# Performance work log

Hardware: AMD Instinct MI355X
Metric: run time of the kernel (lower is better)

Reference implementation:

```python
import jax, jax.numpy as jnp
import numpy as np

B, N, F_IN, F_OUT, H = 4, 2048, 64, 64, 4

def setup_inputs() -> dict:
    key = jax.random.key(0)
    k1, k2, k3, k4 = jax.random.split(key, 4)
    node_features = jax.random.normal(k1, (B, N, F_IN), dtype=jnp.float32)
    adj_matrix = jax.random.randint(k2, (B, N, N), 0, 2, dtype=jnp.int32)
    # nn.Linear(in, H*out, bias=False): stored here as [in, H*out] so y = x @ W
    W = jax.random.normal(k3, (F_IN, H * F_OUT), dtype=jnp.float32) * (1.0 / np.sqrt(F_IN))
    # per-head additive-attention vector over concatenated [h_i || h_j] (width 2*F_OUT)
    attention = jax.random.normal(k4, (H, 2 * F_OUT), dtype=jnp.float32) * 0.1
    return {"node_features": node_features, "adj_matrix": adj_matrix, "W": W, "attention": attention}

def reference(node_features, adj_matrix, W, attention):
    Bv, Nv = node_features.shape[0], node_features.shape[1]
    # h: [B, H, N, F_OUT]
    h = (node_features @ W).reshape(Bv, Nv, H, F_OUT).transpose(0, 2, 1, 3)
    # Additive GAT scores: a_h . [h_i || h_j] decomposed so the [B,H,N,N,2F] concat
    # tensor is never materialized (same math as concat + einsum in the source).
    a_src, a_dst = attention[:, :F_OUT], attention[:, F_OUT:]
    s_src = jnp.einsum('bhnf,hf->bhn', h, a_src)
    s_dst = jnp.einsum('bhnf,hf->bhn', h, a_dst)
    scores = s_src[:, :, :, None] + s_dst[:, :, None, :]          # [B,H,N,N]
    scores = jnp.where(scores >= 0, scores, 0.2 * scores)          # LeakyReLU(0.2)
    mask = adj_matrix[:, None, :, :].astype(bool)                  # [B,1,N,N]
    scores = jnp.where(mask, scores, -jnp.inf)                     # masked_fill(~mask, -inf)
    attn = jax.nn.softmax(scores, axis=-1)                         # softmax over neighbors j
    # dropout is identity in eval mode (deterministic reference)
    h_prime = jnp.einsum('bhij,bhjf->bhif', attn, h)               # weighted neighbor sum
    return h_prime.transpose(0, 2, 1, 3).reshape(Bv, Nv, H * F_OUT)
```

## Files before the change

kernel.cpp:

```cpp
#include <hip/hip_runtime.h>

#define NN 2048
#define NH 4
#define COLS 256

typedef __attribute__((ext_vector_type(8))) short short8;
typedef __attribute__((ext_vector_type(4))) float f32x4;
typedef __attribute__((ext_vector_type(4))) int i32x4;
typedef __attribute__((ext_vector_type(4))) unsigned u32x4;

__device__ __forceinline__ ushort f2bf(float x) {
  union { float f; unsigned u; } v; v.f = x;
  unsigned r = v.u + 0x7fffu + ((v.u >> 16) & 1u);
  return (ushort)(r >> 16);
}
__device__ __forceinline__ unsigned cvtpk(float lo, float hi) {
  unsigned r;
  asm("v_cvt_pk_bf16_f32 %0, %1, %2" : "=v"(r) : "v"(lo), "v"(hi));
  return r;
}
__device__ __forceinline__ unsigned pack16(i32x4 a, i32x4 b, i32x4 c, i32x4 d) {
  unsigned m = 0;
  #pragma unroll
  for (int e = 0; e < 4; ++e) {
    m |= (a[e] != 0 ? 1u : 0u) << e;
    m |= (b[e] != 0 ? 1u : 0u) << (e + 4);
    m |= (c[e] != 0 ? 1u : 0u) << (e + 8);
    m |= (d[e] != 0 ? 1u : 0u) << (e + 12);
  }
  return m;
}

__global__ __launch_bounds__(256) void k1_prep(
    const float* __restrict__ nf, const float* __restrict__ W,
    const float* __restrict__ att, ushort* __restrict__ hB,
    float* __restrict__ s_src, float* __restrict__ s_dst)
{
  const int tid = threadIdx.x;
  const int head = tid >> 6, lane = tid & 63;
  const int bid = blockIdx.x;

  float w[64];
  #pragma unroll
  for (int f = 0; f < 64; ++f) w[f] = W[f * COLS + tid];

  const float LOG2E = 1.4426950408889634f;
  const float asrc = att[head * 128 + lane] * LOG2E;
  const float adst = att[head * 128 + 64 + lane] * LOG2E;

  __shared__ float xs[512];
  __shared__ ushort st8[8 * 256];

  #pragma unroll 1
  for (int g = 0; g < 2; ++g) {
    const int m0 = bid * 16 + g * 8;
    __syncthreads();
    xs[tid]       = nf[m0 * 64 + tid];
    xs[tid + 256] = nf[m0 * 64 + 256 + tid];
    __syncthreads();

    #pragma unroll
    for (int rr = 0; rr < 8; ++rr) {
      float acc = 0.f;
      #pragma unroll
      for (int f = 0; f < 64; ++f) acc = fmaf(xs[rr * 64 + f], w[f], acc);
      st8[rr * 256 + tid] = f2bf(acc);
      float vs = acc * asrc, vd = acc * adst;
      #pragma unroll
      for (int off = 32; off > 0; off >>= 1) {
        vs += __shfl_xor(vs, off);
        vd += __shfl_xor(vd, off);
      }
      if (lane == 0) {
        const int m = m0 + rr;
        const int b = m >> 11, n = m & (NN - 1);
        s_src[(b * NH + head) * NN + n] = vs;
        s_dst[(b * NH + head) * NN + n] = vd;
      }
    }
    __syncthreads();
    {
      const int t = (tid >> 4) & 3, fl = tid & 15;
      const int col = head * 64 + t * 16 + fl;
      unsigned pk[4];
      #pragma unroll
      for (int e = 0; e < 4; ++e) {
        const unsigned lo = st8[(2 * e) * 256 + col];
        const unsigned hi = st8[(2 * e + 1) * 256 + col];
        pk[e] = lo | (hi << 16);
      }
      const int b   = m0 >> 11;
      const int jc  = (m0 & (NN - 1)) >> 5;
      const int grp = (m0 & 31) >> 3;
      const size_t chunk =
          (((size_t)(b * NH + head) * 64 + jc) * 4 + t) * 64 + (grp * 16 + fl);
      uint4 vv; vv.x = pk[0]; vv.y = pk[1]; vv.z = pk[2]; vv.w = pk[3];
      *(uint4*)(hB + chunk * 8) = vv;
    }
  }
}

__global__ __launch_bounds__(1024) void k2_main(
    const int* __restrict__ adj, const ushort* __restrict__ hB,
    const float* __restrict__ s_src, const float* __restrict__ s_dst,
    float* __restrict__ out)
{
  const int tid = threadIdx.x;
  const int wv  = tid >> 6;
  const int w   = wv >> 2;
  const int js  = wv & 3;
  const int l   = tid & 63;
  int bid = blockIdx.x;
  bid = (bid & 7) * 32 + (bid >> 3);
  const int b   = bid >> 6;
  const int i0  = (bid & 63) << 5;

  const int bh   = b * NH + w;
  const int r16  = l & 15;
  const int grp  = l >> 4;
  const int koff = grp << 3;

  const int sjs = tid >> 8, srow = (tid >> 3) & 31, soct = tid & 7;
  const int* sbase = adj + ((size_t)b * NN + i0 + srow) * NN + sjs * 512 + soct * 16;

  const float ssl = s_src[bh * NN + i0 + r16];
  const float ssh = s_src[bh * NN + i0 + 16 + r16];
  const float*  sdp = s_dst + bh * NN;
  const ushort* hbW = hB + (size_t)bh * 131072 + l * 8;

  __shared__ unsigned abits[2][4][32][4];
  __shared__ f32x4 red[NH][10][64];

  const short8 ones = {(short)0x3F80, (short)0x3F80, (short)0x3F80, (short)0x3F80,
                       (short)0x3F80, (short)0x3F80, (short)0x3F80, (short)0x3F80};

  f32x4 acc[8];
  #pragma unroll
  for (int q = 0; q < 8; ++q) acc[q] = (f32x4){0.f, 0.f, 0.f, 0.f};
  f32x4 acd0 = (f32x4){0.f, 0.f, 0.f, 0.f};
  f32x4 acd1 = (f32x4){0.f, 0.f, 0.f, 0.f};

  {
    const i32x4 ra0 = *(const i32x4*)(sbase + 0);
    const i32x4 ra1 = *(const i32x4*)(sbase + 4);
    const i32x4 ra2 = *(const i32x4*)(sbase + 8);
    const i32x4 ra3 = *(const i32x4*)(sbase + 12);
    ushort* p = (ushort*)&abits[0][sjs][srow][0];
    p[soct] = (ushort)pack16(ra0, ra1, ra2, ra3);
  }
  __syncthreads();

  #pragma unroll 1
  for (int s = 0; s < 4; ++s) {
    i32x4 ra0, ra1, ra2, ra3;
    if (s < 3) {
      const int* sp = sbase + (s + 1) * 128;
      ra0 = *(const i32x4*)(sp + 0);
      ra1 = *(const i32x4*)(sp + 4);
      ra2 = *(const i32x4*)(sp + 8);
      ra3 = *(const i32x4*)(sp + 12);
    }
    const int cur = s & 1;

    #pragma unroll
    for (int q4 = 0; q4 < 4; ++q4) {
      const int jc = js * 16 + s * 4 + q4;
      const unsigned wlo = abits[cur][js][r16][q4];
      const unsigned whi = abits[cur][js][r16 + 16][q4];
      const int jb = jc * 32 + koff;
      const f32x4 sd0 = *(const f32x4*)(sdp + jb);
      const f32x4 sd1 = *(const f32x4*)(sdp + jb + 4);
      const ushort* hc = hbW + jc * 2048;
      const short8 hb0 = *(const short8*)(hc);
      const short8 hb1 = *(const short8*)(hc + 512);
      const short8 hb2 = *(const short8*)(hc + 1024);
      const short8 hb3 = *(const short8*)(hc + 1536);

      float pl[8], ph[8];
      #pragma unroll
      for (int e = 0; e < 8; ++e) {
        const float sdv = (e < 4) ? sd0[e] : sd1[e - 4];
        float x = ssl + sdv;
        x = fmaxf(x, 0.2f * x);
        const float p = __builtin_amdgcn_exp2f(x);
        pl[e] = ((wlo >> (koff + e)) & 1u) ? p : 0.f;
        float y = ssh + sdv;
        y = fmaxf(y, 0.2f * y);
        const float qv = __builtin_amdgcn_exp2f(y);
        ph[e] = ((whi >> (koff + e)) & 1u) ? qv : 0.f;
      }
      u32x4 pa, pb;
      #pragma unroll
      for (int e2 = 0; e2 < 4; ++e2) {
        pa[e2] = cvtpk(pl[2 * e2], pl[2 * e2 + 1]);
        pb[e2] = cvtpk(ph[2 * e2], ph[2 * e2 + 1]);
      }
      union { u32x4 u; short8 s; } ca, cb;
      ca.u = pa; cb.u = pb;
      const short8 pal = ca.s, pah = cb.s;

      acc[0] = __builtin_amdgcn_mfma_f32_16x16x32_bf16(pal, hb0, acc[0], 0, 0, 0);
      acc[1] = __builtin_amdgcn_mfma_f32_16x16x32_bf16(pal, hb1, acc[1], 0, 0, 0);
      acc[2] = __builtin_amdgcn_mfma_f32_16x16x32_bf16(pal, hb2, acc[2], 0, 0, 0);
      acc[3] = __builtin_amdgcn_mfma_f32_16x16x32_bf16(pal, hb3, acc[3], 0, 0, 0);
      acc[4] = __builtin_amdgcn_mfma_f32_16x16x32_bf16(pah, hb0, acc[4], 0, 0, 0);
      acc[5] = __builtin_amdgcn_mfma_f32_16x16x32_bf16(pah, hb1, acc[5], 0, 0, 0);
      acc[6] = __builtin_amdgcn_mfma_f32_16x16x32_bf16(pah, hb2, acc[6], 0, 0, 0);
      acc[7] = __builtin_amdgcn_mfma_f32_16x16x32_bf16(pah, hb3, acc[7], 0, 0, 0);
      acd0   = __builtin_amdgcn_mfma_f32_16x16x32_bf16(pal, ones, acd0, 0, 0, 0);
      acd1   = __builtin_amdgcn_mfma_f32_16x16x32_bf16(pah, ones, acd1, 0, 0, 0);
    }

    if (s < 3) {
      ushort* p = (ushort*)&abits[cur ^ 1][sjs][srow][0];
      p[soct] = (ushort)pack16(ra0, ra1, ra2, ra3);
    }
    __syncthreads();
  }

  #pragma unroll 1
  for (int st = 1; st < 4; ++st) {
    if (js == st) {
      #pragma unroll
      for (int q = 0; q < 8; ++q) red[w][q][l] = acc[q];
      red[w][8][l] = acd0;
      red[w][9][l] = acd1;
    }
    __syncthreads();
    if (js == 0) {
      #pragma unroll
      for (int q = 0; q < 8; ++q) acc[q] += red[w][q][l];
      acd0 += red[w][8][l];
      acd1 += red[w][9][l];
    }
    __syncthreads();
  }

  if (js == 0) {
    float rl[4], rh[4];
    #pragma unroll
    for (int r = 0; r < 4; ++r) { rl[r] = 1.0f / acd0[r]; rh[r] = 1.0f / acd1[r]; }
    #pragma unroll
    for (int sx = 0; sx < 2; ++sx) {
      #pragma unroll
      for (int t = 0; t < 4; ++t) {
        const f32x4 a = acc[sx * 4 + t];
        #pragma unroll
        for (int r = 0; r < 4; ++r) {
          const int i = i0 + sx * 16 + grp * 4 + r;
          const size_t oidx = ((size_t)(b * NN + i) * COLS) + w * 64 + t * 16 + r16;
          out[oidx] = a[r] * (sx ? rh[r] : rl[r]);
        }
      }
    }
  }
}

extern "C" void kernel_launch(void* const* d_in, const int* in_sizes, int n_in,
                              void* d_out, int out_size, void* d_ws, size_t ws_size,
                              hipStream_t stream) {
  const float* nf  = (const float*)d_in[0];
  const int*   adj = (const int*)d_in[1];
  const float* W   = (const float*)d_in[2];
  const float* att = (const float*)d_in[3];

  ushort* hB    = (ushort*)d_ws;
  float*  s_src = (float*)((char*)d_ws + (size_t)16 * 64 * NN * 2);
  float*  s_dst = s_src + 16 * NN;

  hipLaunchKernelGGL(k1_prep, dim3(512), dim3(256), 0, stream,
                     nf, W, att, hB, s_src, s_dst);
  hipLaunchKernelGGL(k2_main, dim3(256), dim3(1024), 0, stream,
                     adj, hB, s_src, s_dst, (float*)d_out);
}
```

Before: 56.42 us.

## Halve row tile in attention kernel to double grid, simplify prep and reduction

The main kernel now processes 16 query rows per block instead of 32, which doubles the grid to 512 blocks and halves the accumulator registers per wave. A launch-bounds occupancy hint is added. The split-K reduction becomes a single shared-memory pass with padded layouts instead of three sequential rounds. The prep kernel handles 8 rows per block with a doubled grid and packs bf16 directly in registers, so the shared-memory staging is gone. The trade-off is that each hB tile and s_dst vector is now read by twice as many blocks, and half the threads sit idle during adjacency loads.

```diff
diff --git a/kernel.cpp b/kernel.cpp
--- a/kernel.cpp
+++ b/kernel.cpp
@@ -9,11 +9,6 @@
 typedef __attribute__((ext_vector_type(4))) int i32x4;
 typedef __attribute__((ext_vector_type(4))) unsigned u32x4;
 
-__device__ __forceinline__ ushort f2bf(float x) {
-  union { float f; unsigned u; } v; v.f = x;
-  unsigned r = v.u + 0x7fffu + ((v.u >> 16) & 1u);
-  return (ushort)(r >> 16);
-}
 __device__ __forceinline__ unsigned cvtpk(float lo, float hi) {
   unsigned r;
   asm("v_cvt_pk_bf16_f32 %0, %1, %2" : "=v"(r) : "v"(lo), "v"(hi));
@@ -39,6 +34,7 @@
   const int tid = threadIdx.x;
   const int head = tid >> 6, lane = tid & 63;
   const int bid = blockIdx.x;
+  const int m0 = bid * 8;
 
   float w[64];
   #pragma unroll
@@ -49,58 +45,47 @@
   const float adst = att[head * 128 + 64 + lane] * LOG2E;
 
   __shared__ float xs[512];
-  __shared__ ushort st8[8 * 256];
-
-  #pragma unroll 1
-  for (int g = 0; g < 2; ++g) {
-    const int m0 = bid * 16 + g * 8;
-    __syncthreads();
-    xs[tid]       = nf[m0 * 64 + tid];
-    xs[tid + 256] = nf[m0 * 64 + 256 + tid];
-    __syncthreads();
-
-    #pragma unroll
-    for (int rr = 0; rr < 8; ++rr) {
-      float acc = 0.f;
-      #pragma unroll
-      for (int f = 0; f < 64; ++f) acc = fmaf(xs[rr * 64 + f], w[f], acc);
-      st8[rr * 256 + tid] = f2bf(acc);
-      float vs = acc * asrc, vd = acc * adst;
-      #pragma unroll
-      for (int off = 32; off > 0; off >>= 1) {
-        vs += __shfl_xor(vs, off);
-        vd += __shfl_xor(vd, off);
-      }
-      if (lane == 0) {
-        const int m = m0 + rr;
-        const int b = m >> 11, n = m & (NN - 1);
-        s_src[(b * NH + head) * NN + n] = vs;
-        s_dst[(b * NH + head) * NN + n] = vd;
-      }
-    }
-    __syncthreads();
-    {
-      const int t = (tid >> 4) & 3, fl = tid & 15;
-      const int col = head * 64 + t * 16 + fl;
-      unsigned pk[4];
-      #pragma unroll
-      for (int e = 0; e < 4; ++e) {
-        const unsigned lo = st8[(2 * e) * 256 + col];
-        const unsigned hi = st8[(2 * e + 1) * 256 + col];
-        pk[e] = lo | (hi << 16);
-      }
-      const int b   = m0 >> 11;
-      const int jc  = (m0 & (NN - 1)) >> 5;
-      const int grp = (m0 & 31) >> 3;
-      const size_t chunk =
-          (((size_t)(b * NH + head) * 64 + jc) * 4 + t) * 64 + (grp * 16 + fl);
-      uint4 vv; vv.x = pk[0]; vv.y = pk[1]; vv.z = pk[2]; vv.w = pk[3];
-      *(uint4*)(hB + chunk * 8) = vv;
-    }
-  }
-}
-
-__global__ __launch_bounds__(1024) void k2_main(
+  xs[tid]       = nf[m0 * 64 + tid];
+  xs[tid + 256] = nf[m0 * 64 + 256 + tid];
+  __syncthreads();
+
+  float hv[8];
+  #pragma unroll
+  for (int rr = 0; rr < 8; ++rr) {
+    float acc = 0.f;
+    #pragma unroll
+    for (int f = 0; f < 64; ++f) acc = fmaf(xs[rr * 64 + f], w[f], acc);
+    hv[rr] = acc;
+    float vs = acc * asrc, vd = acc * adst;
+    #pragma unroll
+    for (int off = 32; off > 0; off >>= 1) {
+      vs += __shfl_xor(vs, off);
+      vd += __shfl_xor(vd, off);
+    }
+    if (lane == 0) {
+      const int m = m0 + rr;
+      const int b = m >> 11, n = m & (NN - 1);
+      s_src[(b * NH + head) * NN + n] = vs;
+      s_dst[(b * NH + head) * NN + n] = vd;
+    }
+  }
+
+  const int b   = m0 >> 11;
+  const int n0  = m0 & (NN - 1);
+  const int jc  = n0 >> 5;
+  const int grp = (n0 >> 3) & 3;
+  const int t   = (tid >> 4) & 3, fl = tid & 15;
+  uint4 vv;
+  vv.x = cvtpk(hv[0], hv[1]);
+  vv.y = cvtpk(hv[2], hv[3]);
+  vv.z = cvtpk(hv[4], hv[5]);
+  vv.w = cvtpk(hv[6], hv[7]);
+  const size_t chunk =
+      (((size_t)(b * NH + head) * 64 + jc) * 4 + t) * 64 + (grp * 16 + fl);
+  *(uint4*)(hB + chunk * 8) = vv;
+}
+
+__global__ __launch_bounds__(1024, 8) void k2_main(
     const int* __restrict__ adj, const ushort* __restrict__ hB,
     const float* __restrict__ s_src, const float* __restrict__ s_dst,
     float* __restrict__ out)
@@ -111,49 +96,46 @@
   const int js  = wv & 3;
   const int l   = tid & 63;
   int bid = blockIdx.x;
-  bid = (bid & 7) * 32 + (bid >> 3);
-  const int b   = bid >> 6;
-  const int i0  = (bid & 63) << 5;
+  bid = (bid & 7) * 64 + (bid >> 3);
+  const int b   = bid >> 7;
+  const int i0  = (bid & 127) << 4;
 
   const int bh   = b * NH + w;
   const int r16  = l & 15;
   const int grp  = l >> 4;
   const int koff = grp << 3;
 
-  const int sjs = tid >> 8, srow = (tid >> 3) & 31, soct = tid & 7;
-  const int* sbase = adj + ((size_t)b * NN + i0 + srow) * NN + sjs * 512 + soct * 16;
-
   const float ssl = s_src[bh * NN + i0 + r16];
-  const float ssh = s_src[bh * NN + i0 + 16 + r16];
   const float*  sdp = s_dst + bh * NN;
   const ushort* hbW = hB + (size_t)bh * 131072 + l * 8;
 
-  __shared__ unsigned abits[2][4][32][4];
-  __shared__ f32x4 red[NH][10][64];
+  const int sjs = tid >> 7, srow = (tid >> 3) & 15, soct = tid & 7;
+  const int* sbase = adj + ((size_t)b * NN + i0 + srow) * NN + sjs * 512 + soct * 16;
+
+  __shared__ unsigned abits[2][4][16][5];
+  __shared__ float red[NH][3][5][4][64];
 
   const short8 ones = {(short)0x3F80, (short)0x3F80, (short)0x3F80, (short)0x3F80,
                        (short)0x3F80, (short)0x3F80, (short)0x3F80, (short)0x3F80};
 
-  f32x4 acc[8];
-  #pragma unroll
-  for (int q = 0; q < 8; ++q) acc[q] = (f32x4){0.f, 0.f, 0.f, 0.f};
-  f32x4 acd0 = (f32x4){0.f, 0.f, 0.f, 0.f};
-  f32x4 acd1 = (f32x4){0.f, 0.f, 0.f, 0.f};
-
-  {
+  f32x4 acc[4];
+  #pragma unroll
+  for (int q = 0; q < 4; ++q) acc[q] = (f32x4){0.f, 0.f, 0.f, 0.f};
+  f32x4 acd = (f32x4){0.f, 0.f, 0.f, 0.f};
+
+  if (tid < 512) {
     const i32x4 ra0 = *(const i32x4*)(sbase + 0);
     const i32x4 ra1 = *(const i32x4*)(sbase + 4);
     const i32x4 ra2 = *(const i32x4*)(sbase + 8);
     const i32x4 ra3 = *(const i32x4*)(sbase + 12);
-    ushort* p = (ushort*)&abits[0][sjs][srow][0];
-    p[soct] = (ushort)pack16(ra0, ra1, ra2, ra3);
+    ((ushort*)&abits[0][sjs][srow][0])[soct] = (ushort)pack16(ra0, ra1, ra2, ra3);
   }
   __syncthreads();
 
   #pragma unroll 1
   for (int s = 0; s < 4; ++s) {
     i32x4 ra0, ra1, ra2, ra3;
-    if (s < 3) {
+    if (s < 3 && tid < 512) {
       const int* sp = sbase + (s + 1) * 128;
       ra0 = *(const i32x4*)(sp + 0);
       ra1 = *(const i32x4*)(sp + 4);
@@ -166,7 +148,6 @@
     for (int q4 = 0; q4 < 4; ++q4) {
       const int jc = js * 16 + s * 4 + q4;
       const unsigned wlo = abits[cur][js][r16][q4];
-      const unsigned whi = abits[cur][js][r16 + 16][q4];
       const int jb = jc * 32 + koff;
       const f32x4 sd0 = *(const f32x4*)(sdp + jb);
       const f32x4 sd1 = *(const f32x4*)(sdp + jb + 4);
@@ -176,7 +157,7 @@
       const short8 hb2 = *(const short8*)(hc + 1024);
       const short8 hb3 = *(const short8*)(hc + 1536);
 
-      float pl[8], ph[8];
+      float pl[8];
       #pragma unroll
       for (int e = 0; e < 8; ++e) {
         const float sdv = (e < 4) ? sd0[e] : sd1[e - 4];
@@ -184,73 +165,55 @@
         x = fmaxf(x, 0.2f * x);
         const float p = __builtin_amdgcn_exp2f(x);
         pl[e] = ((wlo >> (koff + e)) & 1u) ? p : 0.f;
-        float y = ssh + sdv;
-        y = fmaxf(y, 0.2f * y);
-        const float qv = __builtin_amdgcn_exp2f(y);
-        ph[e] = ((whi >> (koff + e)) & 1u) ? qv : 0.f;
       }
-      u32x4 pa, pb;
-      #pragma unroll
-      for (int e2 = 0; e2 < 4; ++e2) {
-        pa[e2] = cvtpk(pl[2 * e2], pl[2 * e2 + 1]);
-        pb[e2] = cvtpk(ph[2 * e2], ph[2 * e2 + 1]);
-      }
-      union { u32x4 u; short8 s; } ca, cb;
-      ca.u = pa; cb.u = pb;
-      const short8 pal = ca.s, pah = cb.s;
+      u32x4 pa;
+      #pragma unroll
+      for (int e2 = 0; e2 < 4; ++e2) pa[e2] = cvtpk(pl[2 * e2], pl[2 * e2 + 1]);
+      union { u32x4 u; short8 s; } ca; ca.u = pa;
+      const short8 pal = ca.s;
 
       acc[0] = __builtin_amdgcn_mfma_f32_16x16x32_bf16(pal, hb0, acc[0], 0, 0, 0);
       acc[1] = __builtin_amdgcn_mfma_f32_16x16x32_bf16(pal, hb1, acc[1], 0, 0, 0);
       acc[2] = __builtin_amdgcn_mfma_f32_16x16x32_bf16(pal, hb2, acc[2], 0, 0, 0);
       acc[3] = __builtin_amdgcn_mfma_f32_16x16x32_bf16(pal, hb3, acc[3], 0, 0, 0);
-      acc[4] = __builtin_amdgcn_mfma_f32_16x16x32_bf16(pah, hb0, acc[4], 0, 0, 0);
-      acc[5] = __builtin_amdgcn_mfma_f32_16x16x32_bf16(pah, hb1, acc[5], 0, 0, 0);
-      acc[6] = __builtin_amdgcn_mfma_f32_16x16x32_bf16(pah, hb2, acc[6], 0, 0, 0);
-      acc[7] = __builtin_amdgcn_mfma_f32_16x16x32_bf16(pah, hb3, acc[7], 0, 0, 0);
-      acd0   = __builtin_amdgcn_mfma_f32_16x16x32_bf16(pal, ones, acd0, 0, 0, 0);
-      acd1   = __builtin_amdgcn_mfma_f32_16x16x32_bf16(pah, ones, acd1, 0, 0, 0);
-    }
-
-    if (s < 3) {
-      ushort* p = (ushort*)&abits[cur ^ 1][sjs][srow][0];
-      p[soct] = (ushort)pack16(ra0, ra1, ra2, ra3);
-    }
+      acd    = __builtin_amdgcn_mfma_f32_16x16x32_bf16(pal, ones, acd,    0, 0, 0);
+    }
+
+    if (s < 3 && tid < 512)
+      ((ushort*)&abits[cur ^ 1][sjs][srow][0])[soct] = (ushort)pack16(ra0, ra1, ra2, ra3);
     __syncthreads();
   }
 
-  #pragma unroll 1
-  for (int st = 1; st < 4; ++st) {
-    if (js == st) {
-      #pragma unroll
-      for (int q = 0; q < 8; ++q) red[w][q][l] = acc[q];
-      red[w][8][l] = acd0;
-      red[w][9][l] = acd1;
-    }
-    __syncthreads();
-    if (js == 0) {
-      #pragma unroll
-      for (int q = 0; q < 8; ++q) acc[q] += red[w][q][l];
-      acd0 += red[w][8][l];
-      acd1 += red[w][9][l];
-    }
-    __syncthreads();
-  }
+  if (js > 0) {
+    #pragma unroll
+    for (int t = 0; t < 4; ++t)
+      #pragma unroll
+      for (int r = 0; r < 4; ++r) red[w][js - 1][t][r][l] = acc[t][r];
+    #pragma unroll
+    for (int r = 0; r < 4; ++r) red[w][js - 1][4][r][l] = acd[r];
+  }
+  __syncthreads();
 
   if (js == 0) {
-    float rl[4], rh[4];
-    #pragma unroll
-    for (int r = 0; r < 4; ++r) { rl[r] = 1.0f / acd0[r]; rh[r] = 1.0f / acd1[r]; }
-    #pragma unroll
-    for (int sx = 0; sx < 2; ++sx) {
-      #pragma unroll
-      for (int t = 0; t < 4; ++t) {
-        const f32x4 a = acc[sx * 4 + t];
+    #pragma unroll
+    for (int src = 0; src < 3; ++src) {
+      #pragma unroll
+      for (int t = 0; t < 4; ++t)
         #pragma unroll
-        for (int r = 0; r < 4; ++r) {
-          const int i = i0 + sx * 16 + grp * 4 + r;
-          const size_t oidx = ((size_t)(b * NN + i) * COLS) + w * 64 + t * 16 + r16;
-          out[oidx] = a[r] * (sx ? rh[r] : rl[r]);
-        }
+        for (int r = 0; r < 4; ++r) acc[t][r] += red[w][src][t][r][l];
+      #pragma unroll
+      for (int r = 0; r < 4; ++r) acd[r] += red[w][src][4][r][l];
+    }
+    float rl[4];
+    #pragma unroll
+    for (int r = 0; r < 4; ++r) rl[r] = 1.0f / acd[r];
+    #pragma unroll
+    for (int t = 0; t < 4; ++t) {
+      #pragma unroll
+      for (int r = 0; r < 4; ++r) {
+        const int i = i0 + grp * 4 + r;
+        const size_t oidx = ((size_t)(b * NN + i) * COLS) + w * 64 + t * 16 + r16;
+        out[oidx] = acc[t][r] * rl[r];
       }
     }
   }
@@ -268,8 +231,8 @@
   float*  s_src = (float*)((char*)d_ws + (size_t)16 * 64 * NN * 2);
   float*  s_dst = s_src + 16 * NN;
 
-  hipLaunchKernelGGL(k1_prep, dim3(512), dim3(256), 0, stream,
+  hipLaunchKernelGGL(k1_prep, dim3(1024), dim3(256), 0, stream,
                      nf, W, att, hB, s_src, s_dst);
-  hipLaunchKernelGGL(k2_main, dim3(256), dim3(1024), 0, stream,
+  hipLaunchKernelGGL(k2_main, dim3(512), dim3(1024), 0, stream,
                      adj, hB, s_src, s_dst, (float*)d_out);
 }
```

After: 78.36 us. 38.9% more time.
